# Kernel optimization log

Hardware: AMD Instinct MI355X
Metric: run time of the kernel (lower is better)

## Reference

```python
import jax, jax.numpy as jnp
import numpy as np

K = 10
ALPHA = 0.1
N_NODES = 100000
N_EDGES = 1600000
IN_DIM = 128
HID_DIM = 128
OUT_DIM = 128


def setup_inputs() -> dict:
    key = jax.random.key(0)
    k_x, k_e, k_w1, k_b1, k_w2, k_b2 = jax.random.split(key, 6)
    x = jax.random.normal(k_x, (N_NODES, IN_DIM), dtype=jnp.float32)
    edge_index = jax.random.randint(k_e, (2, N_EDGES), 0, N_NODES, dtype=jnp.int64)
    # Linear params (Kaiming-uniform-ish scale, exact init irrelevant for correctness)
    s1 = 1.0 / np.sqrt(IN_DIM)
    s2 = 1.0 / np.sqrt(HID_DIM)
    W1 = jax.random.uniform(k_w1, (IN_DIM, HID_DIM), jnp.float32, -s1, s1)
    b1 = jax.random.uniform(k_b1, (HID_DIM,), jnp.float32, -s1, s1)
    W2 = jax.random.uniform(k_w2, (HID_DIM, OUT_DIM), jnp.float32, -s2, s2)
    b2 = jax.random.uniform(k_b2, (OUT_DIM,), jnp.float32, -s2, s2)
    return {"x": x, "edge_index": edge_index, "W1": W1, "b1": b1, "W2": W2, "b2": b2}


def reference(x, edge_index, W1, b1, W2, b2):
    n = x.shape[0]
    h = jax.nn.relu(x @ W1 + b1)  # [N, H]

    # gcn_norm: add self loops, symmetric normalization D^-1/2 (A+I) D^-1/2
    loop = jnp.arange(n, dtype=edge_index.dtype)
    src = jnp.concatenate([edge_index[0], loop])  # [E+N]
    dst = jnp.concatenate([edge_index[1], loop])  # [E+N]
    ones = jnp.ones(src.shape[0], dtype=h.dtype)
    deg = jax.ops.segment_sum(ones, dst, num_segments=n)  # [N]
    dinv = jnp.where(deg > 0, jax.lax.rsqrt(deg), 0.0)
    norm = (dinv[src] * dinv[dst])[:, None]  # [E+N, 1]

    # APPNP: K steps of h = (1-alpha) * A_hat h + alpha * h0
    h0 = h

    def step(h, _):
        msg = norm * h[src]  # gather + scale  [E+N, H]
        agg = jax.ops.segment_sum(msg, dst, num_segments=n)  # scatter-add [N, H]
        return (1.0 - ALPHA) * agg + ALPHA * h0, None

    h, _ = jax.lax.scan(step, h, None, length=K)
    return h @ W2 + b2
```

## Files before the change

### kernel.cpp

```cpp
#include <hip/hip_runtime.h>
#include <stdint.h>

#define N_NODES 100000
#define N_EDGES 1600000
#define HDIM    128
#define KSTEPS  10
#define NZONE   8
#define ZDIV    12500u

typedef unsigned int uint;

#define SCAN_T     256
#define SCAN_I     4
#define SCAN_ELEMS (SCAN_T * SCAN_I)
#define SCAN_NB    ((N_NODES + SCAN_ELEMS - 1) / SCAN_ELEMS)

__device__ inline float2 bf2_to_f2(uint v) {
    float2 r;
    r.x = __uint_as_float(v << 16);
    r.y = __uint_as_float(v & 0xffff0000u);
    return r;
}
__device__ inline uint f_to_bf_bits(float f) {
    uint u = __float_as_uint(f);
    return (u + 0x7fffu + ((u >> 16) & 1u)) >> 16;
}
__device__ inline uint f2_to_bf2(float x, float y) {
    return f_to_bf_bits(x) | (f_to_bf_bits(y) << 16);
}

__global__ void k_countpos(const int* __restrict__ eidx, int* __restrict__ cnt,
                           int* __restrict__ pos) {
    int e0 = (blockIdx.x * blockDim.x + threadIdx.x) * 4;
    if (e0 < N_EDGES) {
        int4 d4 = *(const int4*)&eidx[N_EDGES + e0];
        int4 p;
        p.x = atomicAdd(&cnt[d4.x], 1);
        p.y = atomicAdd(&cnt[d4.y], 1);
        p.z = atomicAdd(&cnt[d4.z], 1);
        p.w = atomicAdd(&cnt[d4.w], 1);
        *(int4*)&pos[e0] = p;
    }
}

__global__ void k_scan1(const int* __restrict__ cnt, int* __restrict__ rp,
                        int* __restrict__ bsum) {
    __shared__ int s[SCAN_T];
    int tid  = threadIdx.x;
    int base = blockIdx.x * SCAN_ELEMS + tid * SCAN_I;
    int v[SCAN_I];
    int loc = 0;
#pragma unroll
    for (int j = 0; j < SCAN_I; ++j) {
        int idx = base + j;
        v[j] = (idx < N_NODES) ? cnt[idx] : 0;
        loc += v[j];
    }
    s[tid] = loc;
    __syncthreads();
    for (int off = 1; off < SCAN_T; off <<= 1) {
        int t = (tid >= off) ? s[tid - off] : 0;
        __syncthreads();
        s[tid] += t;
        __syncthreads();
    }
    int run = s[tid] - loc;
#pragma unroll
    for (int j = 0; j < SCAN_I; ++j) {
        int idx = base + j;
        if (idx < N_NODES) rp[idx] = run;
        run += v[j];
    }
    if (tid == SCAN_T - 1) bsum[blockIdx.x] = s[SCAN_T - 1];
}

__global__ void k_scan2(const int* __restrict__ bsum, int* __restrict__ boff,
                        int* __restrict__ rp) {
    int acc = 0;
    for (int i = 0; i < SCAN_NB; ++i) { boff[i] = acc; acc += bsum[i]; }
    rp[N_NODES] = acc;
}

__global__ void k_scan3(int* __restrict__ rp, const int* __restrict__ boff) {
    int off = boff[blockIdx.x];
#pragma unroll
    for (int j = 0; j < SCAN_I; ++j) {
        int i = blockIdx.x * SCAN_ELEMS + threadIdx.x + j * SCAN_T;
        if (i < N_NODES) rp[i] += off;
    }
}

__global__ void k_dinv(const int* __restrict__ cnt, float* __restrict__ dinv,
                       float* __restrict__ dsq) {
    int i = blockIdx.x * blockDim.x + threadIdx.x;
    if (i < N_NODES) {
        float d = 1.0f + (float)cnt[i];
        dinv[i] = rsqrtf(d);
        dsq[i]  = sqrtf(d);
    }
}

#define FCHUNK 8192
#define FECH   ((N_EDGES + FCHUNK - 1) / FCHUNK)
__global__ __launch_bounds__(256)
void k_fill2(const int* __restrict__ eidx, const int* __restrict__ rp,
             const int* __restrict__ pos, int* __restrict__ col) {
    uint zone = blockIdx.x;
    int  base = blockIdx.y * FCHUNK;
#pragma unroll
    for (int i = 0; i < FCHUNK / 1024; ++i) {
        int e0 = base + (i * 256 + (int)threadIdx.x) * 4;
        if (e0 < N_EDGES) {
            int4 d4 = *(const int4*)&eidx[N_EDGES + e0];
            int4 s4 = *(const int4*)&eidx[e0];
            int4 p4 = *(const int4*)&pos[e0];
            if ((uint)d4.x / ZDIV == zone) col[rp[d4.x] + p4.x] = s4.x;
            if ((uint)d4.y / ZDIV == zone) col[rp[d4.y] + p4.y] = s4.y;
            if ((uint)d4.z / ZDIV == zone) col[rp[d4.z] + p4.z] = s4.z;
            if ((uint)d4.w / ZDIV == zone) col[rp[d4.w] + p4.w] = s4.w;
        }
    }
}

#define KCH 64
__global__ __launch_bounds__(256)
void k_gemm1(const float* __restrict__ x, const float* __restrict__ W,
             const float* __restrict__ bias, const float* __restrict__ dinv,
             uint* __restrict__ out) {
    __shared__ __align__(16) float wlds[KCH][HDIM];
    __shared__ __align__(16) float xs[32][KCH + 1];
    int tid  = threadIdx.x;
    int tx   = tid & 31, ty = tid >> 5;
    int row0 = blockIdx.x * 32;

    float4 bc = *(const float4*)&bias[tx * 4];

    float acc[4][4] = {};
    for (int kc = 0; kc < HDIM; kc += KCH) {
#pragma unroll
        for (int i = 0; i < 8; ++i) {
            int id = tid + i * 256;
            int kk = id >> 5, n4 = id & 31;
            *(float4*)&wlds[kk][n4 * 4] =
                *(const float4*)&W[(size_t)(kc + kk) * HDIM + n4 * 4];
        }
#pragma unroll
        for (int i = 0; i < 2; ++i) {
            int id = tid + i * 256;
            int r = id >> 4, c4 = id & 15;
            float4 v = *(const float4*)&x[(size_t)(row0 + r) * HDIM + kc + c4 * 4];
            xs[r][c4 * 4 + 0] = v.x;
            xs[r][c4 * 4 + 1] = v.y;
            xs[r][c4 * 4 + 2] = v.z;
            xs[r][c4 * 4 + 3] = v.w;
        }
        __syncthreads();
#pragma unroll 8
        for (int kk = 0; kk < KCH; ++kk) {
            float4 b4 = *(const float4*)&wlds[kk][tx * 4];
            float a0 = xs[ty * 4 + 0][kk];
            float a1 = xs[ty * 4 + 1][kk];
            float a2 = xs[ty * 4 + 2][kk];
            float a3 = xs[ty * 4 + 3][kk];
            acc[0][0] += a0 * b4.x; acc[0][1] += a0 * b4.y; acc[0][2] += a0 * b4.z; acc[0][3] += a0 * b4.w;
            acc[1][0] += a1 * b4.x; acc[1][1] += a1 * b4.y; acc[1][2] += a1 * b4.z; acc[1][3] += a1 * b4.w;
            acc[2][0] += a2 * b4.x; acc[2][1] += a2 * b4.y; acc[2][2] += a2 * b4.z; acc[2][3] += a2 * b4.w;
            acc[3][0] += a3 * b4.x; acc[3][1] += a3 * b4.y; acc[3][2] += a3 * b4.z; acc[3][3] += a3 * b4.w;
        }
        __syncthreads();
    }
#pragma unroll
    for (int r = 0; r < 4; ++r) {
        int row = row0 + ty * 4 + r;
        float di = dinv[row];
        float v0 = fmaxf(acc[r][0] + bc.x, 0.0f) * di;
        float v1 = fmaxf(acc[r][1] + bc.y, 0.0f) * di;
        float v2 = fmaxf(acc[r][2] + bc.z, 0.0f) * di;
        float v3 = fmaxf(acc[r][3] + bc.w, 0.0f) * di;
        uint2 p;
        p.x = f2_to_bf2(v0, v1);
        p.y = f2_to_bf2(v2, v3);
        *(uint2*)&out[(size_t)row * 64 + tx * 2] = p;
    }
}

__global__ __launch_bounds__(256)
void k_gemm2(const uint* __restrict__ u, const float* __restrict__ W,
             const float* __restrict__ bias, const float* __restrict__ dsq,
             float* __restrict__ out) {
    __shared__ __align__(16) float wlds[KCH][HDIM];
    __shared__ __align__(16) float xs[32][KCH + 1];
    int tid  = threadIdx.x;
    int tx   = tid & 31, ty = tid >> 5;
    int row0 = blockIdx.x * 32;

    float4 bc = *(const float4*)&bias[tx * 4];

    float acc[4][4] = {};
    for (int kc = 0; kc < HDIM; kc += KCH) {
#pragma unroll
        for (int i = 0; i < 8; ++i) {
            int id = tid + i * 256;
            int kk = id >> 5, n4 = id & 31;
            *(float4*)&wlds[kk][n4 * 4] =
                *(const float4*)&W[(size_t)(kc + kk) * HDIM + n4 * 4];
        }
#pragma unroll
        for (int i = 0; i < 2; ++i) {
            int id = tid + i * 256;
            int r = id >> 4, c4 = id & 15;
            float ds = dsq[row0 + r];
            uint2 v = *(const uint2*)&u[(size_t)(row0 + r) * 64 + (kc >> 1) + c4 * 2];
            float2 f0 = bf2_to_f2(v.x);
            float2 f1 = bf2_to_f2(v.y);
            xs[r][c4 * 4 + 0] = f0.x * ds;
            xs[r][c4 * 4 + 1] = f0.y * ds;
            xs[r][c4 * 4 + 2] = f1.x * ds;
            xs[r][c4 * 4 + 3] = f1.y * ds;
        }
        __syncthreads();
#pragma unroll 8
        for (int kk = 0; kk < KCH; ++kk) {
            float4 b4 = *(const float4*)&wlds[kk][tx * 4];
            float a0 = xs[ty * 4 + 0][kk];
            float a1 = xs[ty * 4 + 1][kk];
            float a2 = xs[ty * 4 + 2][kk];
            float a3 = xs[ty * 4 + 3][kk];
            acc[0][0] += a0 * b4.x; acc[0][1] += a0 * b4.y; acc[0][2] += a0 * b4.z; acc[0][3] += a0 * b4.w;
            acc[1][0] += a1 * b4.x; acc[1][1] += a1 * b4.y; acc[1][2] += a1 * b4.z; acc[1][3] += a1 * b4.w;
            acc[2][0] += a2 * b4.x; acc[2][1] += a2 * b4.y; acc[2][2] += a2 * b4.z; acc[2][3] += a2 * b4.w;
            acc[3][0] += a3 * b4.x; acc[3][1] += a3 * b4.y; acc[3][2] += a3 * b4.z; acc[3][3] += a3 * b4.w;
        }
        __syncthreads();
    }
#pragma unroll
    for (int r = 0; r < 4; ++r) {
        int row = row0 + ty * 4 + r;
        float4 v;
        v.x = acc[r][0] + bc.x;
        v.y = acc[r][1] + bc.y;
        v.z = acc[r][2] + bc.z;
        v.w = acc[r][3] + bc.w;
        *(float4*)&out[(size_t)row * HDIM + tx * 4] = v;
    }
}

__global__ __launch_bounds__(256)
void k_step(const uint* __restrict__ uin, const uint* __restrict__ u0,
            uint* __restrict__ uout, const int* __restrict__ col,
            const int* __restrict__ rp, const float* __restrict__ dinv) {
    int wid  = (blockIdx.x * blockDim.x + threadIdx.x) >> 6;
    int node = __builtin_amdgcn_readfirstlane(wid);
    int lane = threadIdx.x & 63;
    if (node >= N_NODES) return;

    size_t self = (size_t)node * 64 + lane;
    uint usv = uin[self];
    uint uzv = __builtin_nontemporal_load(&u0[self]);
    float di = dinv[node];
    float w  = 0.9f * di * di;

    int beg = rp[node], end = rp[node + 1];
    float2 us = bf2_to_f2(usv);
    float accx = us.x, accy = us.y;

    int e = beg;
    for (; e + 8 <= end; e += 8) {
        int s0 = col[e + 0], s1 = col[e + 1], s2 = col[e + 2], s3 = col[e + 3];
        int s4 = col[e + 4], s5 = col[e + 5], s6 = col[e + 6], s7 = col[e + 7];
        uint b0 = uin[(size_t)s0 * 64 + lane];
        uint b1 = uin[(size_t)s1 * 64 + lane];
        uint b2 = uin[(size_t)s2 * 64 + lane];
        uint b3 = uin[(size_t)s3 * 64 + lane];
        uint b4 = uin[(size_t)s4 * 64 + lane];
        uint b5 = uin[(size_t)s5 * 64 + lane];
        uint b6 = uin[(size_t)s6 * 64 + lane];
        uint b7 = uin[(size_t)s7 * 64 + lane];
        float2 a0 = bf2_to_f2(b0), a1 = bf2_to_f2(b1);
        float2 a2 = bf2_to_f2(b2), a3 = bf2_to_f2(b3);
        float2 a4 = bf2_to_f2(b4), a5 = bf2_to_f2(b5);
        float2 a6 = bf2_to_f2(b6), a7 = bf2_to_f2(b7);
        accx += ((a0.x + a1.x) + (a2.x + a3.x)) + ((a4.x + a5.x) + (a6.x + a7.x));
        accy += ((a0.y + a1.y) + (a2.y + a3.y)) + ((a4.y + a5.y) + (a6.y + a7.y));
    }
    if (e + 4 <= end) {
        int s0 = col[e], s1 = col[e + 1], s2 = col[e + 2], s3 = col[e + 3];
        uint b0 = uin[(size_t)s0 * 64 + lane];
        uint b1 = uin[(size_t)s1 * 64 + lane];
        uint b2 = uin[(size_t)s2 * 64 + lane];
        uint b3 = uin[(size_t)s3 * 64 + lane];
        float2 a0 = bf2_to_f2(b0), a1 = bf2_to_f2(b1);
        float2 a2 = bf2_to_f2(b2), a3 = bf2_to_f2(b3);
        accx += (a0.x + a1.x) + (a2.x + a3.x);
        accy += (a0.y + a1.y) + (a2.y + a3.y);
        e += 4;
    }
    if (e + 2 <= end) {
        int s0 = col[e], s1 = col[e + 1];
        uint b0 = uin[(size_t)s0 * 64 + lane];
        uint b1 = uin[(size_t)s1 * 64 + lane];
        float2 a0 = bf2_to_f2(b0), a1 = bf2_to_f2(b1);
        accx += a0.x + a1.x;
        accy += a0.y + a1.y;
        e += 2;
    }
    if (e < end) {
        uint b0 = uin[(size_t)col[e] * 64 + lane];
        float2 a0 = bf2_to_f2(b0);
        accx += a0.x;
        accy += a0.y;
    }
    float2 uz = bf2_to_f2(uzv);
    float ox = w * accx + 0.1f * uz.x;
    float oy = w * accy + 0.1f * uz.y;
    __builtin_nontemporal_store(f2_to_bf2(ox, oy), &uout[self]);
}

extern "C" void kernel_launch(void* const* d_in, const int* in_sizes, int n_in,
                              void* d_out, int out_size, void* d_ws, size_t ws_size,
                              hipStream_t stream) {
    (void)in_sizes; (void)n_in; (void)out_size; (void)ws_size;
    const float* x  = (const float*)d_in[0];
    const int*   ei = (const int*)d_in[1];
    const float* W1 = (const float*)d_in[2];
    const float* b1 = (const float*)d_in[3];
    const float* W2 = (const float*)d_in[4];
    const float* b2 = (const float*)d_in[5];
    float* out = (float*)d_out;

    char* ws = (char*)d_ws;
    size_t off = 0;
    auto alloc = [&](size_t bytes) -> void* {
        void* p = ws + off;
        off += (bytes + 255) & ~(size_t)255;
        return p;
    };
    uint*  u0   = (uint*)alloc(sizeof(uint) * (size_t)N_NODES * 64);
    uint*  uA   = (uint*)alloc(sizeof(uint) * (size_t)N_NODES * 64);
    uint*  uB   = (uint*)alloc(sizeof(uint) * (size_t)N_NODES * 64);
    int*   col  = (int*)alloc(sizeof(int) * N_EDGES);
    int*   pos  = (int*)alloc(sizeof(int) * N_EDGES);
    int*   rp   = (int*)alloc(sizeof(int) * (N_NODES + 1));
    int*   cnt  = (int*)alloc(sizeof(int) * N_NODES);
    float* dinv = (float*)alloc(sizeof(float) * N_NODES);
    float* dsq  = (float*)alloc(sizeof(float) * N_NODES);
    int*   bsum = (int*)alloc(sizeof(int) * SCAN_NB);
    int*   boff = (int*)alloc(sizeof(int) * SCAN_NB);

    hipMemsetAsync(cnt, 0, sizeof(int) * N_NODES, stream);

    k_countpos<<<(N_EDGES / 4 + 255) / 256, 256, 0, stream>>>(ei, cnt, pos);
    k_scan1<<<SCAN_NB, SCAN_T, 0, stream>>>(cnt, rp, bsum);
    k_scan2<<<1, 1, 0, stream>>>(bsum, boff, rp);
    k_scan3<<<SCAN_NB, SCAN_T, 0, stream>>>(rp, boff);
    k_dinv<<<(N_NODES + 255) / 256, 256, 0, stream>>>(cnt, dinv, dsq);
    {
        dim3 g(NZONE, FECH);
        k_fill2<<<g, 256, 0, stream>>>(ei, rp, pos, col);
    }

    k_gemm1<<<N_NODES / 32, 256, 0, stream>>>(x, W1, b1, dinv, u0);

    const uint* uin = u0;
    uint* uout = uA;
    for (int k = 0; k < KSTEPS; ++k) {
        k_step<<<N_NODES / 4, 256, 0, stream>>>(uin, u0, uout, col, rp, dinv);
        uin = uout;
        uout = (uout == uA) ? uB : uA;
    }
    k_gemm2<<<N_NODES / 32, 256, 0, stream>>>(uin, W2, b2, dsq, out);
}
```

Before: 924.2 us.

## Bin CSR edges by source zone and process 16 nodes per wavefront

Each destination node's edges are now bucketed by source-node zone (8 zones), producing a zone-major CSR over 800k bins. The scan is widened to cover them, and the second scan pass is parallelized. The propagation kernel gives each wavefront 16 destination nodes and walks the zones in order, keeping 4 interleaved gather streams in flight, so gathers from the feature table stay within a smaller source range. This is meant to improve cache locality for the random gathers. In exchange it adds preprocessing work, reduces the number of waves, and brings divergent per-node loops and load imbalance. Scratch arrays now reuse the ping-pong buffers.

```diff
diff --git a/kernel.cpp b/kernel.cpp
--- a/kernel.cpp
+++ b/kernel.cpp
@@ -8,12 +8,17 @@
 #define NZONE   8
 #define ZDIV    12500u
 
+#define NZS     8
+#define SZDIV   12500u
+#define NBINS   (NZS * N_NODES)
+
 typedef unsigned int uint;
 
 #define SCAN_T     256
 #define SCAN_I     4
 #define SCAN_ELEMS (SCAN_T * SCAN_I)
-#define SCAN_NB    ((N_NODES + SCAN_ELEMS - 1) / SCAN_ELEMS)
+#define SCAN_NB    ((NBINS + SCAN_ELEMS - 1) / SCAN_ELEMS)
+#define S2_I       4
 
 __device__ inline float2 bf2_to_f2(uint v) {
     float2 r;
@@ -33,12 +38,13 @@
                            int* __restrict__ pos) {
     int e0 = (blockIdx.x * blockDim.x + threadIdx.x) * 4;
     if (e0 < N_EDGES) {
+        int4 s4 = *(const int4*)&eidx[e0];
         int4 d4 = *(const int4*)&eidx[N_EDGES + e0];
         int4 p;
-        p.x = atomicAdd(&cnt[d4.x], 1);
-        p.y = atomicAdd(&cnt[d4.y], 1);
-        p.z = atomicAdd(&cnt[d4.z], 1);
-        p.w = atomicAdd(&cnt[d4.w], 1);
+        p.x = atomicAdd(&cnt[(int)((uint)s4.x / SZDIV) * N_NODES + d4.x], 1);
+        p.y = atomicAdd(&cnt[(int)((uint)s4.y / SZDIV) * N_NODES + d4.y], 1);
+        p.z = atomicAdd(&cnt[(int)((uint)s4.z / SZDIV) * N_NODES + d4.z], 1);
+        p.w = atomicAdd(&cnt[(int)((uint)s4.w / SZDIV) * N_NODES + d4.w], 1);
         *(int4*)&pos[e0] = p;
     }
 }
@@ -53,7 +59,7 @@
 #pragma unroll
     for (int j = 0; j < SCAN_I; ++j) {
         int idx = base + j;
-        v[j] = (idx < N_NODES) ? cnt[idx] : 0;
+        v[j] = (idx < NBINS) ? cnt[idx] : 0;
         loc += v[j];
     }
     s[tid] = loc;
@@ -68,7 +74,7 @@
 #pragma unroll
     for (int j = 0; j < SCAN_I; ++j) {
         int idx = base + j;
-        if (idx < N_NODES) rp[idx] = run;
+        if (idx < NBINS) rp[idx] = run;
         run += v[j];
     }
     if (tid == SCAN_T - 1) bsum[blockIdx.x] = s[SCAN_T - 1];
@@ -76,9 +82,32 @@
 
 __global__ void k_scan2(const int* __restrict__ bsum, int* __restrict__ boff,
                         int* __restrict__ rp) {
-    int acc = 0;
-    for (int i = 0; i < SCAN_NB; ++i) { boff[i] = acc; acc += bsum[i]; }
-    rp[N_NODES] = acc;
+    __shared__ int s[SCAN_T];
+    int tid = threadIdx.x;
+    int v[S2_I];
+    int loc = 0;
+#pragma unroll
+    for (int j = 0; j < S2_I; ++j) {
+        int idx = tid * S2_I + j;
+        v[j] = (idx < SCAN_NB) ? bsum[idx] : 0;
+        loc += v[j];
+    }
+    s[tid] = loc;
+    __syncthreads();
+    for (int off = 1; off < SCAN_T; off <<= 1) {
+        int t = (tid >= off) ? s[tid - off] : 0;
+        __syncthreads();
+        s[tid] += t;
+        __syncthreads();
+    }
+    int run = s[tid] - loc;
+#pragma unroll
+    for (int j = 0; j < S2_I; ++j) {
+        int idx = tid * S2_I + j;
+        if (idx < SCAN_NB) boff[idx] = run;
+        run += v[j];
+    }
+    if (tid == SCAN_T - 1) rp[NBINS] = s[SCAN_T - 1];
 }
 
 __global__ void k_scan3(int* __restrict__ rp, const int* __restrict__ boff) {
@@ -86,15 +115,19 @@
 #pragma unroll
     for (int j = 0; j < SCAN_I; ++j) {
         int i = blockIdx.x * SCAN_ELEMS + threadIdx.x + j * SCAN_T;
-        if (i < N_NODES) rp[i] += off;
-    }
-}
-
-__global__ void k_dinv(const int* __restrict__ cnt, float* __restrict__ dinv,
+        if (i < NBINS) rp[i] += off;
+    }
+}
+
+__global__ void k_dinv(const int* __restrict__ rpz, float* __restrict__ dinv,
                        float* __restrict__ dsq) {
     int i = blockIdx.x * blockDim.x + threadIdx.x;
     if (i < N_NODES) {
-        float d = 1.0f + (float)cnt[i];
+        int deg = 0;
+#pragma unroll
+        for (int z = 0; z < NZS; ++z)
+            deg += rpz[(size_t)z * N_NODES + i + 1] - rpz[(size_t)z * N_NODES + i];
+        float d = 1.0f + (float)deg;
         dinv[i] = rsqrtf(d);
         dsq[i]  = sqrtf(d);
     }
@@ -103,7 +136,7 @@
 #define FCHUNK 8192
 #define FECH   ((N_EDGES + FCHUNK - 1) / FCHUNK)
 __global__ __launch_bounds__(256)
-void k_fill2(const int* __restrict__ eidx, const int* __restrict__ rp,
+void k_fill2(const int* __restrict__ eidx, const int* __restrict__ rpz,
              const int* __restrict__ pos, int* __restrict__ col) {
     uint zone = blockIdx.x;
     int  base = blockIdx.y * FCHUNK;
@@ -114,10 +147,14 @@
             int4 d4 = *(const int4*)&eidx[N_EDGES + e0];
             int4 s4 = *(const int4*)&eidx[e0];
             int4 p4 = *(const int4*)&pos[e0];
-            if ((uint)d4.x / ZDIV == zone) col[rp[d4.x] + p4.x] = s4.x;
-            if ((uint)d4.y / ZDIV == zone) col[rp[d4.y] + p4.y] = s4.y;
-            if ((uint)d4.z / ZDIV == zone) col[rp[d4.z] + p4.z] = s4.z;
-            if ((uint)d4.w / ZDIV == zone) col[rp[d4.w] + p4.w] = s4.w;
+            if ((uint)d4.x / ZDIV == zone)
+                col[rpz[(int)((uint)s4.x / SZDIV) * N_NODES + d4.x] + p4.x] = s4.x;
+            if ((uint)d4.y / ZDIV == zone)
+                col[rpz[(int)((uint)s4.y / SZDIV) * N_NODES + d4.y] + p4.y] = s4.y;
+            if ((uint)d4.z / ZDIV == zone)
+                col[rpz[(int)((uint)s4.z / SZDIV) * N_NODES + d4.z] + p4.z] = s4.z;
+            if ((uint)d4.w / ZDIV == zone)
+                col[rpz[(int)((uint)s4.w / SZDIV) * N_NODES + d4.w] + p4.w] = s4.w;
         }
     }
 }
@@ -245,75 +282,60 @@
     }
 }
 
-__global__ __launch_bounds__(256)
-void k_step(const uint* __restrict__ uin, const uint* __restrict__ u0,
+#define JPW 16
+__global__ __launch_bounds__(256, 6)
+void k_prop(const uint* __restrict__ uin, const uint* __restrict__ u0,
             uint* __restrict__ uout, const int* __restrict__ col,
-            const int* __restrict__ rp, const float* __restrict__ dinv) {
-    int wid  = (blockIdx.x * blockDim.x + threadIdx.x) >> 6;
-    int node = __builtin_amdgcn_readfirstlane(wid);
+            const int* __restrict__ rpz, const float* __restrict__ dinv) {
+    int wid  = __builtin_amdgcn_readfirstlane((int)(blockIdx.x * 4 + (threadIdx.x >> 6)));
     int lane = threadIdx.x & 63;
-    if (node >= N_NODES) return;
-
-    size_t self = (size_t)node * 64 + lane;
-    uint usv = uin[self];
-    uint uzv = __builtin_nontemporal_load(&u0[self]);
-    float di = dinv[node];
-    float w  = 0.9f * di * di;
-
-    int beg = rp[node], end = rp[node + 1];
-    float2 us = bf2_to_f2(usv);
-    float accx = us.x, accy = us.y;
-
-    int e = beg;
-    for (; e + 8 <= end; e += 8) {
-        int s0 = col[e + 0], s1 = col[e + 1], s2 = col[e + 2], s3 = col[e + 3];
-        int s4 = col[e + 4], s5 = col[e + 5], s6 = col[e + 6], s7 = col[e + 7];
-        uint b0 = uin[(size_t)s0 * 64 + lane];
-        uint b1 = uin[(size_t)s1 * 64 + lane];
-        uint b2 = uin[(size_t)s2 * 64 + lane];
-        uint b3 = uin[(size_t)s3 * 64 + lane];
-        uint b4 = uin[(size_t)s4 * 64 + lane];
-        uint b5 = uin[(size_t)s5 * 64 + lane];
-        uint b6 = uin[(size_t)s6 * 64 + lane];
-        uint b7 = uin[(size_t)s7 * 64 + lane];
-        float2 a0 = bf2_to_f2(b0), a1 = bf2_to_f2(b1);
-        float2 a2 = bf2_to_f2(b2), a3 = bf2_to_f2(b3);
-        float2 a4 = bf2_to_f2(b4), a5 = bf2_to_f2(b5);
-        float2 a6 = bf2_to_f2(b6), a7 = bf2_to_f2(b7);
-        accx += ((a0.x + a1.x) + (a2.x + a3.x)) + ((a4.x + a5.x) + (a6.x + a7.x));
-        accy += ((a0.y + a1.y) + (a2.y + a3.y)) + ((a4.y + a5.y) + (a6.y + a7.y));
-    }
-    if (e + 4 <= end) {
-        int s0 = col[e], s1 = col[e + 1], s2 = col[e + 2], s3 = col[e + 3];
-        uint b0 = uin[(size_t)s0 * 64 + lane];
-        uint b1 = uin[(size_t)s1 * 64 + lane];
-        uint b2 = uin[(size_t)s2 * 64 + lane];
-        uint b3 = uin[(size_t)s3 * 64 + lane];
-        float2 a0 = bf2_to_f2(b0), a1 = bf2_to_f2(b1);
-        float2 a2 = bf2_to_f2(b2), a3 = bf2_to_f2(b3);
-        accx += (a0.x + a1.x) + (a2.x + a3.x);
-        accy += (a0.y + a1.y) + (a2.y + a3.y);
-        e += 4;
-    }
-    if (e + 2 <= end) {
-        int s0 = col[e], s1 = col[e + 1];
-        uint b0 = uin[(size_t)s0 * 64 + lane];
-        uint b1 = uin[(size_t)s1 * 64 + lane];
-        float2 a0 = bf2_to_f2(b0), a1 = bf2_to_f2(b1);
-        accx += a0.x + a1.x;
-        accy += a0.y + a1.y;
-        e += 2;
-    }
-    if (e < end) {
-        uint b0 = uin[(size_t)col[e] * 64 + lane];
-        float2 a0 = bf2_to_f2(b0);
-        accx += a0.x;
-        accy += a0.y;
-    }
-    float2 uz = bf2_to_f2(uzv);
-    float ox = w * accx + 0.1f * uz.x;
-    float oy = w * accy + 0.1f * uz.y;
-    __builtin_nontemporal_store(f2_to_bf2(ox, oy), &uout[self]);
+    int n0   = wid * JPW;
+    if (n0 >= N_NODES) return;
+
+    float ax[JPW], ay[JPW];
+#pragma unroll
+    for (int j = 0; j < JPW; ++j) { ax[j] = 0.0f; ay[j] = 0.0f; }
+
+    for (int z = 0; z < NZS; ++z) {
+        const int* bp = &rpz[(size_t)z * N_NODES + n0];
+        int B[JPW + 1];
+#pragma unroll
+        for (int i = 0; i <= JPW; ++i) B[i] = bp[i];
+#pragma unroll
+        for (int g = 0; g < JPW / 4; ++g) {
+            int ea = B[4 * g + 0], Ea = B[4 * g + 1];
+            int eb = B[4 * g + 1], Eb = B[4 * g + 2];
+            int ec = B[4 * g + 2], Ec = B[4 * g + 3];
+            int ed = B[4 * g + 3], Ed = B[4 * g + 4];
+            while ((ea < Ea) | (eb < Eb) | (ec < Ec) | (ed < Ed)) {
+                bool pa = ea < Ea, pb = eb < Eb, pc = ec < Ec, pd = ed < Ed;
+                uint ba, bb, bc, bd;
+                if (pa) ba = uin[(size_t)col[ea] * 64 + lane];
+                if (pb) bb = uin[(size_t)col[eb] * 64 + lane];
+                if (pc) bc = uin[(size_t)col[ec] * 64 + lane];
+                if (pd) bd = uin[(size_t)col[ed] * 64 + lane];
+                if (pa) { float2 f = bf2_to_f2(ba); ax[4*g+0] += f.x; ay[4*g+0] += f.y; ++ea; }
+                if (pb) { float2 f = bf2_to_f2(bb); ax[4*g+1] += f.x; ay[4*g+1] += f.y; ++eb; }
+                if (pc) { float2 f = bf2_to_f2(bc); ax[4*g+2] += f.x; ay[4*g+2] += f.y; ++ec; }
+                if (pd) { float2 f = bf2_to_f2(bd); ax[4*g+3] += f.x; ay[4*g+3] += f.y; ++ed; }
+            }
+        }
+    }
+
+#pragma unroll
+    for (int j = 0; j < JPW; ++j) {
+        int n = n0 + j;
+        size_t self = (size_t)n * 64 + lane;
+        uint usv = uin[self];
+        uint uzv = __builtin_nontemporal_load(&u0[self]);
+        float di = dinv[n];
+        float w  = 0.9f * di * di;
+        float2 us = bf2_to_f2(usv);
+        float2 uz = bf2_to_f2(uzv);
+        float ox = w * (ax[j] + us.x) + 0.1f * uz.x;
+        float oy = w * (ay[j] + us.y) + 0.1f * uz.y;
+        __builtin_nontemporal_store(f2_to_bf2(ox, oy), &uout[self]);
+    }
 }
 
 extern "C" void kernel_launch(void* const* d_in, const int* in_sizes, int n_in,
@@ -339,32 +361,33 @@
     uint*  uA   = (uint*)alloc(sizeof(uint) * (size_t)N_NODES * 64);
     uint*  uB   = (uint*)alloc(sizeof(uint) * (size_t)N_NODES * 64);
     int*   col  = (int*)alloc(sizeof(int) * N_EDGES);
-    int*   pos  = (int*)alloc(sizeof(int) * N_EDGES);
-    int*   rp   = (int*)alloc(sizeof(int) * (N_NODES + 1));
-    int*   cnt  = (int*)alloc(sizeof(int) * N_NODES);
+    int*   rpz  = (int*)alloc(sizeof(int) * (NBINS + 1));
     float* dinv = (float*)alloc(sizeof(float) * N_NODES);
     float* dsq  = (float*)alloc(sizeof(float) * N_NODES);
     int*   bsum = (int*)alloc(sizeof(int) * SCAN_NB);
     int*   boff = (int*)alloc(sizeof(int) * SCAN_NB);
-
-    hipMemsetAsync(cnt, 0, sizeof(int) * N_NODES, stream);
-
-    k_countpos<<<(N_EDGES / 4 + 255) / 256, 256, 0, stream>>>(ei, cnt, pos);
-    k_scan1<<<SCAN_NB, SCAN_T, 0, stream>>>(cnt, rp, bsum);
-    k_scan2<<<1, 1, 0, stream>>>(bsum, boff, rp);
-    k_scan3<<<SCAN_NB, SCAN_T, 0, stream>>>(rp, boff);
-    k_dinv<<<(N_NODES + 255) / 256, 256, 0, stream>>>(cnt, dinv, dsq);
+    int*   cnt2 = (int*)uA;
+    int*   pos  = (int*)uB;
+
+    hipMemsetAsync(cnt2, 0, sizeof(int) * NBINS, stream);
+
+    k_countpos<<<(N_EDGES / 4 + 255) / 256, 256, 0, stream>>>(ei, cnt2, pos);
+    k_scan1<<<SCAN_NB, SCAN_T, 0, stream>>>(cnt2, rpz, bsum);
+    k_scan2<<<1, SCAN_T, 0, stream>>>(bsum, boff, rpz);
+    k_scan3<<<SCAN_NB, SCAN_T, 0, stream>>>(rpz, boff);
+    k_dinv<<<(N_NODES + 255) / 256, 256, 0, stream>>>(rpz, dinv, dsq);
     {
         dim3 g(NZONE, FECH);
-        k_fill2<<<g, 256, 0, stream>>>(ei, rp, pos, col);
+        k_fill2<<<g, 256, 0, stream>>>(ei, rpz, pos, col);
     }
 
     k_gemm1<<<N_NODES / 32, 256, 0, stream>>>(x, W1, b1, dinv, u0);
 
     const uint* uin = u0;
     uint* uout = uA;
+    int nblk = (N_NODES / JPW + 3) / 4;
     for (int k = 0; k < KSTEPS; ++k) {
-        k_step<<<N_NODES / 4, 256, 0, stream>>>(uin, u0, uout, col, rp, dinv);
+        k_prop<<<nblk, 256, 0, stream>>>(uin, u0, uout, col, rpz, dinv);
         uin = uout;
         uout = (uout == uA) ? uB : uA;
     }
```

Result: slower. 1.366 ms (+47.8%).

## Bucket CSR neighbor lists by source zone to improve gather locality

Applied to the files above, without the earlier changes.

The CSR build now counts edges per (destination, source-zone) bin, giving 8 bins per node. As a result, each node's neighbor list is grouped by source-node range, and the per-edge pos array is gone. The aim is better cache locality for the uin gathers in the 10 propagation steps, since neighboring columns come from the same region of the feature array. The cost is a scan over 800k bins instead of 100k, which is why scan2 becomes a parallel block scan. The build also needs extra atomics in the fill pass, and it reuses uA and uB as count scratch.

```diff
diff --git a/kernel.cpp b/kernel.cpp
--- a/kernel.cpp
+++ b/kernel.cpp
@@ -8,12 +8,17 @@
 #define NZONE   8
 #define ZDIV    12500u
 
+#define NZS     8
+#define SZDIV   12500u
+#define NBINS   (N_NODES * NZS)
+
 typedef unsigned int uint;
 
 #define SCAN_T     256
 #define SCAN_I     4
 #define SCAN_ELEMS (SCAN_T * SCAN_I)
-#define SCAN_NB    ((N_NODES + SCAN_ELEMS - 1) / SCAN_ELEMS)
+#define SCAN_NB    ((NBINS + SCAN_ELEMS - 1) / SCAN_ELEMS)
+#define S2_I       4
 
 __device__ inline float2 bf2_to_f2(uint v) {
     float2 r;
@@ -29,17 +34,27 @@
     return f_to_bf_bits(x) | (f_to_bf_bits(y) << 16);
 }
 
-__global__ void k_countpos(const int* __restrict__ eidx, int* __restrict__ cnt,
-                           int* __restrict__ pos) {
-    int e0 = (blockIdx.x * blockDim.x + threadIdx.x) * 4;
-    if (e0 < N_EDGES) {
-        int4 d4 = *(const int4*)&eidx[N_EDGES + e0];
-        int4 p;
-        p.x = atomicAdd(&cnt[d4.x], 1);
-        p.y = atomicAdd(&cnt[d4.y], 1);
-        p.z = atomicAdd(&cnt[d4.z], 1);
-        p.w = atomicAdd(&cnt[d4.w], 1);
-        *(int4*)&pos[e0] = p;
+#define FCHUNK 8192
+#define FECH   ((N_EDGES + FCHUNK - 1) / FCHUNK)
+__global__ __launch_bounds__(256)
+void k_count(const int* __restrict__ eidx, int* __restrict__ cnt) {
+    uint zone = blockIdx.x;
+    int  base = blockIdx.y * FCHUNK;
+#pragma unroll
+    for (int i = 0; i < FCHUNK / 1024; ++i) {
+        int e0 = base + (i * 256 + (int)threadIdx.x) * 4;
+        if (e0 < N_EDGES) {
+            int4 d4 = *(const int4*)&eidx[N_EDGES + e0];
+            int4 s4 = *(const int4*)&eidx[e0];
+            if ((uint)d4.x / ZDIV == zone)
+                atomicAdd(&cnt[d4.x * NZS + (int)((uint)s4.x / SZDIV)], 1);
+            if ((uint)d4.y / ZDIV == zone)
+                atomicAdd(&cnt[d4.y * NZS + (int)((uint)s4.y / SZDIV)], 1);
+            if ((uint)d4.z / ZDIV == zone)
+                atomicAdd(&cnt[d4.z * NZS + (int)((uint)s4.z / SZDIV)], 1);
+            if ((uint)d4.w / ZDIV == zone)
+                atomicAdd(&cnt[d4.w * NZS + (int)((uint)s4.w / SZDIV)], 1);
+        }
     }
 }
 
@@ -53,7 +68,7 @@
 #pragma unroll
     for (int j = 0; j < SCAN_I; ++j) {
         int idx = base + j;
-        v[j] = (idx < N_NODES) ? cnt[idx] : 0;
+        v[j] = (idx < NBINS) ? cnt[idx] : 0;
         loc += v[j];
     }
     s[tid] = loc;
@@ -68,7 +83,7 @@
 #pragma unroll
     for (int j = 0; j < SCAN_I; ++j) {
         int idx = base + j;
-        if (idx < N_NODES) rp[idx] = run;
+        if (idx < NBINS) rp[idx] = run;
         run += v[j];
     }
     if (tid == SCAN_T - 1) bsum[blockIdx.x] = s[SCAN_T - 1];
@@ -76,9 +91,32 @@
 
 __global__ void k_scan2(const int* __restrict__ bsum, int* __restrict__ boff,
                         int* __restrict__ rp) {
-    int acc = 0;
-    for (int i = 0; i < SCAN_NB; ++i) { boff[i] = acc; acc += bsum[i]; }
-    rp[N_NODES] = acc;
+    __shared__ int s[SCAN_T];
+    int tid = threadIdx.x;
+    int v[S2_I];
+    int loc = 0;
+#pragma unroll
+    for (int j = 0; j < S2_I; ++j) {
+        int idx = tid * S2_I + j;
+        v[j] = (idx < SCAN_NB) ? bsum[idx] : 0;
+        loc += v[j];
+    }
+    s[tid] = loc;
+    __syncthreads();
+    for (int off = 1; off < SCAN_T; off <<= 1) {
+        int t = (tid >= off) ? s[tid - off] : 0;
+        __syncthreads();
+        s[tid] += t;
+        __syncthreads();
+    }
+    int run = s[tid] - loc;
+#pragma unroll
+    for (int j = 0; j < S2_I; ++j) {
+        int idx = tid * S2_I + j;
+        if (idx < SCAN_NB) boff[idx] = run;
+        run += v[j];
+    }
+    if (tid == SCAN_T - 1) rp[NBINS] = s[SCAN_T - 1];
 }
 
 __global__ void k_scan3(int* __restrict__ rp, const int* __restrict__ boff) {
@@ -86,25 +124,24 @@
 #pragma unroll
     for (int j = 0; j < SCAN_I; ++j) {
         int i = blockIdx.x * SCAN_ELEMS + threadIdx.x + j * SCAN_T;
-        if (i < N_NODES) rp[i] += off;
-    }
-}
-
-__global__ void k_dinv(const int* __restrict__ cnt, float* __restrict__ dinv,
+        if (i < NBINS) rp[i] += off;
+    }
+}
+
+__global__ void k_dinv(const int* __restrict__ rp, float* __restrict__ dinv,
                        float* __restrict__ dsq) {
     int i = blockIdx.x * blockDim.x + threadIdx.x;
     if (i < N_NODES) {
-        float d = 1.0f + (float)cnt[i];
+        int deg = rp[(i + 1) * NZS] - rp[i * NZS];
+        float d = 1.0f + (float)deg;
         dinv[i] = rsqrtf(d);
         dsq[i]  = sqrtf(d);
     }
 }
 
-#define FCHUNK 8192
-#define FECH   ((N_EDGES + FCHUNK - 1) / FCHUNK)
 __global__ __launch_bounds__(256)
-void k_fill2(const int* __restrict__ eidx, const int* __restrict__ rp,
-             const int* __restrict__ pos, int* __restrict__ col) {
+void k_fill(const int* __restrict__ eidx, const int* __restrict__ rp,
+            int* __restrict__ cntf, int* __restrict__ col) {
     uint zone = blockIdx.x;
     int  base = blockIdx.y * FCHUNK;
 #pragma unroll
@@ -113,11 +150,26 @@
         if (e0 < N_EDGES) {
             int4 d4 = *(const int4*)&eidx[N_EDGES + e0];
             int4 s4 = *(const int4*)&eidx[e0];
-            int4 p4 = *(const int4*)&pos[e0];
-            if ((uint)d4.x / ZDIV == zone) col[rp[d4.x] + p4.x] = s4.x;
-            if ((uint)d4.y / ZDIV == zone) col[rp[d4.y] + p4.y] = s4.y;
-            if ((uint)d4.z / ZDIV == zone) col[rp[d4.z] + p4.z] = s4.z;
-            if ((uint)d4.w / ZDIV == zone) col[rp[d4.w] + p4.w] = s4.w;
+            if ((uint)d4.x / ZDIV == zone) {
+                int b = d4.x * NZS + (int)((uint)s4.x / SZDIV);
+                int p = atomicAdd(&cntf[b], 1);
+                col[rp[b] + p] = s4.x;
+            }
+            if ((uint)d4.y / ZDIV == zone) {
+                int b = d4.y * NZS + (int)((uint)s4.y / SZDIV);
+                int p = atomicAdd(&cntf[b], 1);
+                col[rp[b] + p] = s4.y;
+            }
+            if ((uint)d4.z / ZDIV == zone) {
+                int b = d4.z * NZS + (int)((uint)s4.z / SZDIV);
+                int p = atomicAdd(&cntf[b], 1);
+                col[rp[b] + p] = s4.z;
+            }
+            if ((uint)d4.w / ZDIV == zone) {
+                int b = d4.w * NZS + (int)((uint)s4.w / SZDIV);
+                int p = atomicAdd(&cntf[b], 1);
+                col[rp[b] + p] = s4.w;
+            }
         }
     }
 }
@@ -260,7 +312,7 @@
     float di = dinv[node];
     float w  = 0.9f * di * di;
 
-    int beg = rp[node], end = rp[node + 1];
+    int beg = rp[node * NZS], end = rp[node * NZS + NZS];
     float2 us = bf2_to_f2(usv);
     float accx = us.x, accy = us.y;
 
@@ -339,24 +391,28 @@
     uint*  uA   = (uint*)alloc(sizeof(uint) * (size_t)N_NODES * 64);
     uint*  uB   = (uint*)alloc(sizeof(uint) * (size_t)N_NODES * 64);
     int*   col  = (int*)alloc(sizeof(int) * N_EDGES);
-    int*   pos  = (int*)alloc(sizeof(int) * N_EDGES);
-    int*   rp   = (int*)alloc(sizeof(int) * (N_NODES + 1));
-    int*   cnt  = (int*)alloc(sizeof(int) * N_NODES);
+    int*   rp   = (int*)alloc(sizeof(int) * (NBINS + 1));
     float* dinv = (float*)alloc(sizeof(float) * N_NODES);
     float* dsq  = (float*)alloc(sizeof(float) * N_NODES);
     int*   bsum = (int*)alloc(sizeof(int) * SCAN_NB);
     int*   boff = (int*)alloc(sizeof(int) * SCAN_NB);
-
-    hipMemsetAsync(cnt, 0, sizeof(int) * N_NODES, stream);
-
-    k_countpos<<<(N_EDGES / 4 + 255) / 256, 256, 0, stream>>>(ei, cnt, pos);
-    k_scan1<<<SCAN_NB, SCAN_T, 0, stream>>>(cnt, rp, bsum);
-    k_scan2<<<1, 1, 0, stream>>>(bsum, boff, rp);
-    k_scan3<<<SCAN_NB, SCAN_T, 0, stream>>>(rp, boff);
-    k_dinv<<<(N_NODES + 255) / 256, 256, 0, stream>>>(cnt, dinv, dsq);
+    int*   cnt  = (int*)uA;
+    int*   cntf = (int*)uB;
+
+    hipMemsetAsync(cnt,  0, sizeof(int) * NBINS, stream);
+    hipMemsetAsync(cntf, 0, sizeof(int) * NBINS, stream);
+
     {
         dim3 g(NZONE, FECH);
-        k_fill2<<<g, 256, 0, stream>>>(ei, rp, pos, col);
+        k_count<<<g, 256, 0, stream>>>(ei, cnt);
+    }
+    k_scan1<<<SCAN_NB, SCAN_T, 0, stream>>>(cnt, rp, bsum);
+    k_scan2<<<1, SCAN_T, 0, stream>>>(bsum, boff, rp);
+    k_scan3<<<SCAN_NB, SCAN_T, 0, stream>>>(rp, boff);
+    k_dinv<<<(N_NODES + 255) / 256, 256, 0, stream>>>(rp, dinv, dsq);
+    {
+        dim3 g(NZONE, FECH);
+        k_fill<<<g, 256, 0, stream>>>(ei, rp, cntf, col);
     }
 
     k_gemm1<<<N_NODES / 32, 256, 0, stream>>>(x, W1, b1, dinv, u0);
```

After: 965.9 us. +4.5%, slower.
